# Performance work log

Hardware: AMD Instinct MI355X
Metric: run time of the kernel (lower is better)

Reference implementation:

```python
import jax, jax.numpy as jnp
import numpy as np

VOCAB, EMBED, TOPICS, NDOCS = 30000, 200, 100, 2048
DT_ALPHA, TW_ALPHA = 3.0, 2.0
EPS_OT = 1e-16   # ETP sinkhorn epsilon
EPS_LOG = 1e-12  # FASTopic self.epsilon
N_SINKHORN_ITERS = 100  # fixed iteration count (original: while err>thr and cpt<max_iter)


def pairwise_sqeuclidean(x, y):
    return (jnp.sum(x * x, axis=1, keepdims=True)
            + jnp.sum(y * y, axis=1)
            - 2.0 * (x @ y.T))


def sinkhorn_etp(x, y, a, b, alpha):
    # Entropic OT between point clouds x:[n,d], y:[m,d]; a:[n,1], b:[m,1] marginals.
    M = pairwise_sqeuclidean(x, y)          # [n, m]
    K = jnp.exp(-alpha * M)                  # Gibbs kernel
    u0 = jnp.full_like(a, 1.0 / a.shape[0])

    def step(carry, _):
        u, _v = carry
        v = b / (K.T @ u + EPS_OT)           # [m,1]
        u = a / (K @ v + EPS_OT)             # [n,1]
        return (u, v), None

    (u, v), _ = jax.lax.scan(step, (u0, jnp.zeros_like(b)), None, length=N_SINKHORN_ITERS)
    transp = u * (K * v.T)                   # [n, m] transport plan
    loss = jnp.sum(transp * M)
    return loss, transp


def setup_inputs() -> dict:
    key = jax.random.key(0)
    k1, k2, k3, k4 = jax.random.split(key, 4)
    # word_embeddings: trunc_normal(std=1) then L2-row-normalize
    we = jax.random.truncated_normal(k1, -2.0, 2.0, (VOCAB, EMBED), jnp.float32)
    we = we / jnp.linalg.norm(we, axis=1, keepdims=True)
    # topic_embeddings: trunc_normal(std=0.1) then L2-row-normalize
    te = 0.1 * jax.random.truncated_normal(k2, -2.0, 2.0, (TOPICS, EMBED), jnp.float32)
    te = te / jnp.linalg.norm(te, axis=1, keepdims=True)
    word_weights = jnp.full((VOCAB, 1), 1.0 / VOCAB, jnp.float32)
    topic_weights = jnp.full((TOPICS, 1), 1.0 / TOPICS, jnp.float32)
    train_bow = jax.random.uniform(k3, (NDOCS, VOCAB), jnp.float32)
    doc_embeddings = jax.random.normal(k4, (NDOCS, EMBED), jnp.float32)
    return {
        "train_bow": train_bow,
        "doc_embeddings": doc_embeddings,
        "word_embeddings": we,
        "topic_embeddings": te,
        "word_weights": word_weights,
        "topic_weights": topic_weights,
    }


def reference(train_bow, doc_embeddings, word_embeddings, topic_embeddings,
              word_weights, topic_weights):
    n_docs = doc_embeddings.shape[0]
    n_topics = topic_embeddings.shape[0]
    # DT_ETP: a uniform over docs, b = softmax(topic_weights)
    a_dt = jnp.full((n_docs, 1), 1.0 / n_docs, doc_embeddings.dtype)
    b_dt = jax.nn.softmax(topic_weights, axis=0)
    loss_DT, transp_DT = sinkhorn_etp(doc_embeddings, topic_embeddings, a_dt, b_dt, DT_ALPHA)
    # TW_ETP: a uniform over topics, b = softmax(word_weights)
    a_tw = jnp.full((n_topics, 1), 1.0 / n_topics, topic_embeddings.dtype)
    b_tw = jax.nn.softmax(word_weights, axis=0)
    loss_TW, transp_TW = sinkhorn_etp(topic_embeddings, word_embeddings, a_tw, b_tw, TW_ALPHA)

    loss_ETP = loss_DT + loss_TW
    theta = transp_DT * n_docs               # [N, K]
    beta = transp_TW * n_topics              # [K, V]
    recon = theta @ beta                     # [N, V]
    loss_DSR = -jnp.mean(jnp.sum(train_bow * jnp.log(recon + EPS_LOG), axis=1))
    loss = loss_DSR + loss_ETP
    return loss, loss_DSR, loss_ETP
```

## Files before the change

### kernel.cpp

```cpp
#include <hip/hip_runtime.h>
#include <math.h>

#define V 30000
#define E 200
#define T 100
#define N 2048
#define NITER 100
#define KSTR 112
#define EPS_OT 1e-16f
#define EPS_LOG 1e-12f

#define OFF_KTW    0
#define OFF_KDT    1680000
#define OFF_WW     1884800
#define OFF_DD     1914800
#define OFF_TT     1916848
#define OFF_PM     1916976
#define OFF_PS     1917104
#define OFF_BTW    1917232
#define OFF_BDT    1947232
#define OFF_ACC    1947360
#define OFF_ACCDT  1957360
#define OFF_VTW    1967360
#define OFF_UDT    1997360
#define OFF_UTW    1999408
#define OFF_VDT    1999536
#define OFF_DBL    1999664
#define OFF_FLAG   1999680
#define OFF_KDTNZ  1999681

#define LOBF(u) __uint_as_float((u) << 16)
#define HIBF(u) __uint_as_float((u) & 0xffff0000u)

__device__ __forceinline__ unsigned short f2bf(float f) {
    unsigned int u = __float_as_uint(f);
    return (unsigned short)((u + 0x7fffu + ((u >> 16) & 1u)) >> 16);
}
__device__ __forceinline__ float bf2f(unsigned short h) {
    return __uint_as_float(((unsigned int)h) << 16);
}

__device__ __forceinline__ float brsum(float x, float* red8) {
    int tid = threadIdx.x;
    for (int o = 32; o; o >>= 1) x += __shfl_down(x, o, 64);
    __syncthreads();
    if ((tid & 63) == 0) red8[tid >> 6] = x;
    __syncthreads();
    return (red8[0] + red8[1]) + (red8[2] + red8[3]);
}

__device__ __forceinline__ void load_krow(const unsigned short* kg, int j, unsigned* ku) {
    const uint4* kp = (const uint4*)(kg + (size_t)j * KSTR);
    #pragma unroll
    for (int i = 0; i < 12; i++) {
        uint4 q = kp[i];
        ku[4*i] = q.x; ku[4*i+1] = q.y; ku[4*i+2] = q.z; ku[4*i+3] = q.w;
    }
    uint2 q2 = *(const uint2*)(((const unsigned*)kp) + 48);
    ku[48] = q2.x; ku[49] = q2.y;
}

__global__ void k_pre(const float* __restrict__ we, const float* __restrict__ de,
                      const float* __restrict__ te, const float* __restrict__ wwgt,
                      const float* __restrict__ twgt, float* ws) {
    __shared__ float red[256];
    int tid = threadIdx.x, b = blockIdx.x;
    int gid = b * 256 + tid;
    if (gid < 2 * NITER * T) ws[OFF_ACC + gid] = 0.f;
    if (gid < 16) ws[OFF_DBL + gid] = 0.f;
    if (gid < 2) ((int*)ws)[OFF_FLAG + gid] = 0;
    {
        int r = gid;
        const float* src = nullptr; float* dst = nullptr; int row = 0;
        if (r < V)              { src = we; dst = ws + OFF_WW; row = r; }
        else if (r < V + N)     { src = de; dst = ws + OFF_DD; row = r - V; }
        else if (r < V + N + T) { src = te; dst = ws + OFF_TT; row = r - V - N; }
        if (src) {
            const float4* p = (const float4*)(src + (size_t)row * E);
            float s = 0.f;
            #pragma unroll 10
            for (int i = 0; i < E / 4; i++) { float4 v = p[i]; s += v.x*v.x + v.y*v.y + v.z*v.z + v.w*v.w; }
            dst[row] = s;
        }
    }
    if (b < 118) {
        int j = gid;
        float w = (j < V) ? wwgt[j] : -INFINITY;
        red[tid] = w; __syncthreads();
        for (int s = 128; s > 0; s >>= 1) { if (tid < s) red[tid] = fmaxf(red[tid], red[tid + s]); __syncthreads(); }
        float m = red[0]; __syncthreads();
        float e = (j < V) ? expf(w - m) : 0.f;
        red[tid] = e; __syncthreads();
        for (int s = 128; s > 0; s >>= 1) { if (tid < s) red[tid] += red[tid + s]; __syncthreads(); }
        if (tid == 0) { ws[OFF_PM + b] = m; ws[OFF_PS + b] = red[0]; }
    } else if (b == 120) {
        float w = (tid < T) ? twgt[tid] : -INFINITY;
        red[tid] = w; __syncthreads();
        for (int s = 128; s > 0; s >>= 1) { if (tid < s) red[tid] = fmaxf(red[tid], red[tid + s]); __syncthreads(); }
        float m = red[0]; __syncthreads();
        float e = (tid < T) ? expf(w - m) : 0.f;
        red[tid] = e; __syncthreads();
        for (int s = 128; s > 0; s >>= 1) { if (tid < s) red[tid] += red[tid + s]; __syncthreads(); }
        if (tid < T) ws[OFF_BDT + tid] = e / red[0];
    }
}

__global__ void k_pre2(const float* __restrict__ wwgt, float* ws) {
    __shared__ float red[128];
    int tid = threadIdx.x, b = blockIdx.x;
    float m = (tid < 118) ? ws[OFF_PM + tid] : -INFINITY;
    if (tid < 128) red[tid] = m;
    __syncthreads();
    for (int s = 64; s > 0; s >>= 1) { if (tid < s) red[tid] = fmaxf(red[tid], red[tid + s]); __syncthreads(); }
    float mw = red[0]; __syncthreads();
    float p = (tid < 118) ? ws[OFF_PS + tid] * expf(ws[OFF_PM + tid] - mw) : 0.f;
    if (tid < 128) red[tid] = p;
    __syncthreads();
    for (int s = 64; s > 0; s >>= 1) { if (tid < s) red[tid] += red[tid + s]; __syncthreads(); }
    float Sw = red[0];
    int j = b * 256 + tid;
    if (j < V) ws[OFF_BTW + j] = expf(wwgt[j] - mw) / Sw;
}

__global__ void k_ktw(const float* __restrict__ we, const float* __restrict__ te, float* ws) {
    __shared__ float wt[8][256];
    __shared__ float tp[8][25];
    __shared__ float tts[25];
    int tid = threadIdx.x;
    int j0 = blockIdx.x * 256;
    int t0 = blockIdx.y * 25;
    int j = j0 + tid;
    int jl = (j < V) ? j : V - 1;
    float acc[25];
    #pragma unroll
    for (int i = 0; i < 25; i++) acc[i] = 0.f;
    if (tid < 25) tts[tid] = ws[OFF_TT + t0 + tid];
    for (int kk = 0; kk < E; kk += 8) {
        #pragma unroll
        for (int k = 0; k < 8; k++) wt[k][tid] = we[(size_t)jl * E + kk + k];
        if (tid < 200) { int i = tid >> 3; int k = tid & 7; tp[k][i] = te[(size_t)(t0 + i) * E + kk + k]; }
        __syncthreads();
        #pragma unroll
        for (int k = 0; k < 8; k++) {
            float w = wt[k][tid];
            #pragma unroll
            for (int i = 0; i < 25; i++) acc[i] += tp[k][i] * w;
        }
        __syncthreads();
    }
    if (j < V) {
        float wwj = ws[OFF_WW + j];
        unsigned short* kg = (unsigned short*)(ws + OFF_KTW);
        #pragma unroll
        for (int i = 0; i < 25; i++) {
            float M = tts[i] + wwj - 2.f * acc[i];
            kg[(size_t)j * KSTR + t0 + i] = f2bf(expf(-2.f * M));
        }
    }
}

__global__ void k_kdt(const float* __restrict__ de, const float* __restrict__ te, float* ws) {
    int gid = blockIdx.x * 256 + threadIdx.x;
    if (gid >= N * T) return;
    int n = gid / T; int t = gid - n * T;
    const float4* dp  = (const float4*)(de + (size_t)n * E);
    const float4* tpp = (const float4*)(te + (size_t)t * E);
    float s = 0.f;
    #pragma unroll 10
    for (int i = 0; i < E / 4; i++) { float4 a = dp[i], b = tpp[i]; s += a.x*b.x + a.y*b.y + a.z*b.z + a.w*b.w; }
    float M = ws[OFF_DD + n] + ws[OFF_TT + t] - 2.f * s;
    float kv = expf(-3.f * M);
    ws[OFF_KDT + gid] = kv;
    unsigned long long m = __ballot(kv != 0.f);
    if (m && (threadIdx.x & 63) == 0) atomicOr(((int*)ws) + OFF_KDTNZ, 1);
}

__global__ void k_it(const float* __restrict__ bow, float* ws, int k) {
    __shared__ float sm[256 * 26];
    __shared__ float pr[256];
    __shared__ float u_sh[100];
    __shared__ float red8[8];
    int tid = threadIdx.x, b = blockIdx.x;

    if (b >= 118 && b < 246) {
        if (k >= 96) return;
        const float4* b4 = (const float4*)bow;
        size_t base = (size_t)k * 160000;
        float s = 0.f;
        for (int i = (b - 118) * 256 + tid; i < 160000; i += 128 * 256) {
            float4 x = b4[base + i]; s += (x.x + x.y) + (x.z + x.w);
        }
        float bs = brsum(s, red8);
        if (tid == 0) atomicAdd((double*)(ws + OFF_DBL) + 3, (double)bs);
        return;
    }

    if (b >= 246) {
        if (((volatile int*)ws)[OFF_KDTNZ] == 0) return;
        int d = (b - 246) * 256 + tid;
        if (tid < T) u_sh[tid] = (k == 0) ? 0.f
            : ws[OFF_BDT + tid] / (ws[OFF_ACCDT + (k - 1) * T + tid] + EPS_OT);
        __syncthreads();
        const float* Kr = ws + OFF_KDT + (size_t)d * T;
        float u;
        if (k == 0) u = 1.f / N;
        else {
            float s = 0.f;
            #pragma unroll 4
            for (int t = 0; t < T; t++) s += Kr[t] * u_sh[t];
            u = (1.f / N) / (s + EPS_OT);
        }
        #pragma unroll
        for (int c = 0; c < 4; c++) {
            #pragma unroll
            for (int i = 0; i < 25; i++) sm[tid * 26 + i] = Kr[25 * c + i] * u;
            __syncthreads();
            int g = tid >> 5, tl = tid & 31;
            float s2 = 0.f;
            if (tl < 25) {
                #pragma unroll 8
                for (int q = 0; q < 32; q++) s2 += sm[(g * 32 + q) * 26 + tl];
            }
            pr[g * 32 + tl] = s2;
            __syncthreads();
            if (tid < 25) {
                float r = 0.f;
                #pragma unroll
                for (int g2 = 0; g2 < 8; g2++) r += pr[g2 * 32 + tid];
                atomicAdd(&ws[OFF_ACCDT + k * T + 25 * c + tid], r);
            }
            __syncthreads();
        }
        return;
    }

    const unsigned short* kg = (const unsigned short*)(ws + OFF_KTW);
    int j = b * 256 + tid;
    bool oob = (j >= V);
    int jc = oob ? V - 1 : j;
    unsigned ku[50];
    load_krow(kg, jc, ku);
    if (oob) {
        #pragma unroll
        for (int q = 0; q < 50; q++) ku[q] = 0;
    }
    if (tid < T) u_sh[tid] = (k == 0) ? 0.01f
        : 0.01f / (ws[OFF_ACC + (k - 1) * T + tid] + EPS_OT);
    __syncthreads();
    float s = 0.f;
    #pragma unroll
    for (int q = 0; q < 50; q++)
        s += LOBF(ku[q]) * u_sh[2 * q] + HIBF(ku[q]) * u_sh[2 * q + 1];
    float v = oob ? 0.f : ws[OFF_BTW + j] / (s + EPS_OT);
    if (k == NITER - 1 && !oob) ws[OFF_VTW + j] = v;
    #pragma unroll
    for (int c = 0; c < 4; c++) {
        #pragma unroll
        for (int i = 0; i < 25; i++) {
            int t = 25 * c + i;
            unsigned w = ku[t >> 1];
            float kt = (t & 1) ? HIBF(w) : LOBF(w);
            sm[tid * 26 + i] = kt * v;
        }
        __syncthreads();
        int g = tid >> 5, tl = tid & 31;
        float s2 = 0.f;
        if (tl < 25) {
            #pragma unroll 8
            for (int q = 0; q < 32; q++) s2 += sm[(g * 32 + q) * 26 + tl];
        }
        pr[g * 32 + tl] = s2;
        __syncthreads();
        if (tid < 25) {
            float r = 0.f;
            #pragma unroll
            for (int g2 = 0; g2 < 8; g2++) r += pr[g2 * 32 + tid];
            atomicAdd(&ws[OFF_ACC + k * T + 25 * c + tid], r);
        }
        __syncthreads();
    }
}

__global__ void k_post(float* ws) {
    __shared__ float u_sh[100];
    __shared__ float red8[8];
    int tid = threadIdx.x, b = blockIdx.x;
    if (b < 118) {
        if (tid < T) {
            float uf = 0.01f / (ws[OFF_ACC + (NITER - 1) * T + tid] + EPS_OT);
            u_sh[tid] = uf;
            if (b == 0) ws[OFF_UTW + tid] = uf;
        }
        __syncthreads();
        int j = b * 256 + tid;
        float lt = 0.f;
        if (j < V) {
            const unsigned short* kg = (const unsigned short*)(ws + OFF_KTW);
            unsigned ku[50];
            load_krow(kg, j, ku);
            float v = ws[OFF_VTW + j];
            #pragma unroll
            for (int q = 0; q < 50; q++) {
                float k0 = LOBF(ku[q]), k1 = HIBF(ku[q]);
                if (k0 > 0.f) lt += u_sh[2 * q]     * k0 * v * (-0.5f * logf(k0));
                if (k1 > 0.f) lt += u_sh[2 * q + 1] * k1 * v * (-0.5f * logf(k1));
            }
        }
        float ltb = brsum(lt, red8);
        if (tid == 0) atomicAdd((double*)(ws + OFF_DBL) + 2, (double)ltb);
    } else {
        if (((volatile int*)ws)[OFF_KDTNZ] == 0) return;
        if (tid < T) {
            float vf = ws[OFF_BDT + tid] / (ws[OFF_ACCDT + (NITER - 1) * T + tid] + EPS_OT);
            u_sh[tid] = vf;
            if (b == 118) ws[OFF_VDT + tid] = vf;
        }
        __syncthreads();
        int d = (b - 118) * 256 + tid;
        const float* Kr = ws + OFF_KDT + (size_t)d * T;
        float s = 0.f;
        #pragma unroll 4
        for (int t = 0; t < T; t++) s += Kr[t] * u_sh[t];
        float u = (1.f / N) / (s + EPS_OT);
        ws[OFF_UDT + d] = u;
        float ld = 0.f; int nz = 0;
        for (int t = 0; t < T; t++) {
            float kv = Kr[t];
            if (kv > 0.f) ld += u * kv * u_sh[t] * (-(1.f / 3.f) * logf(kv));
            if ((float)N * u * kv * u_sh[t] != 0.f) nz = 1;
        }
        float ldb = brsum(ld, red8);
        if (tid == 0) atomicAdd((double*)(ws + OFF_DBL) + 1, (double)ldb);
        if (nz) atomicOr(((int*)ws) + OFF_FLAG, 1);
    }
}

__global__ void k_dsr(const float* __restrict__ bow, float* ws) {
    if (*(volatile int*)(((int*)ws) + OFF_FLAG) == 0) return;
    __shared__ float th[32 * T];
    __shared__ float u2[T];
    __shared__ float vd[T];
    __shared__ float red[256];
    __shared__ int flag;
    int tid = threadIdx.x;
    int j0 = blockIdx.x * 256;
    int d0 = blockIdx.y * 32;
    if (tid < T) { vd[tid] = ws[OFF_VDT + tid]; u2[tid] = ws[OFF_UTW + tid]; }
    if (tid == 0) flag = 0;
    __syncthreads();
    bool nz = false;
    for (int idx = tid; idx < 32 * T; idx += 256) {
        int dl = idx / T; int t = idx - dl * T;
        float thv = (float)N * ws[OFF_UDT + d0 + dl] * ws[OFF_KDT + (size_t)(d0 + dl) * T + t] * vd[t];
        th[idx] = thv;
        nz |= (thv != 0.f);
    }
    if (nz) flag = 1;
    __syncthreads();
    int j = j0 + tid;
    float part = 0.f;
    const unsigned short* kg = (const unsigned short*)(ws + OFF_KTW);
    if (flag) {
        float acc[32];
        #pragma unroll
        for (int d = 0; d < 32; d++) acc[d] = 0.f;
        if (j < V) {
            float vj = ws[OFF_VTW + j];
            for (int t = 0; t < T; t++) {
                float kv = bf2f(kg[(size_t)j * KSTR + t]);
                float beta = (float)T * u2[t] * kv * vj;
                #pragma unroll
                for (int d = 0; d < 32; d++) acc[d] += th[d * T + t] * beta;
            }
            for (int d = 0; d < 32; d++)
                part += bow[(size_t)(d0 + d) * V + j] * logf(acc[d] + EPS_LOG);
        }
    } else {
        if (j < V) {
            float sb = 0.f;
            #pragma unroll 8
            for (int d = 0; d < 32; d++) sb += bow[(size_t)(d0 + d) * V + j];
            part = sb * logf(EPS_LOG);
        }
    }
    red[tid] = part; __syncthreads();
    for (int s = 128; s > 0; s >>= 1) { if (tid < s) red[tid] += red[tid + s]; __syncthreads(); }
    if (tid == 0) atomicAdd((double*)(ws + OFF_DBL) + 0, (double)red[0]);
}

__global__ void k_finish(float* ws, float* out) {
    if (threadIdx.x == 0 && blockIdx.x == 0) {
        double* dbl = (double*)(ws + OFF_DBL);
        int flag = ((int*)ws)[OFF_FLAG];
        double dsr_sum = flag ? dbl[0] : dbl[3] * (double)logf(EPS_LOG);
        double ldsr = -dsr_sum / (double)N;
        double letp = dbl[1] + dbl[2];
        out[0] = (float)(ldsr + letp);
        out[1] = (float)ldsr;
        out[2] = (float)letp;
    }
}

extern "C" void kernel_launch(void* const* d_in, const int* in_sizes, int n_in,
                              void* d_out, int out_size, void* d_ws, size_t ws_size,
                              hipStream_t stream) {
    const float* bow  = (const float*)d_in[0];
    const float* de   = (const float*)d_in[1];
    const float* we   = (const float*)d_in[2];
    const float* te   = (const float*)d_in[3];
    const float* wwgt = (const float*)d_in[4];
    const float* twgt = (const float*)d_in[5];
    float* out = (float*)d_out;
    float* ws  = (float*)d_ws;

    k_pre<<<128, 256, 0, stream>>>(we, de, te, wwgt, twgt, ws);
    k_pre2<<<118, 256, 0, stream>>>(wwgt, ws);
    k_ktw<<<dim3(118, 4), 256, 0, stream>>>(we, te, ws);
    k_kdt<<<800, 256, 0, stream>>>(de, te, ws);
    for (int k = 0; k < NITER; k++)
        k_it<<<254, 256, 0, stream>>>(bow, ws, k);
    k_post<<<126, 256, 0, stream>>>(ws);
    k_dsr<<<dim3(118, 64), 256, 0, stream>>>(bow, ws);
    k_finish<<<1, 64, 0, stream>>>(ws, out);
}
```

Baseline: 1.314 ms.

## Fuse Sinkhorn iterations into one persistent kernel with grid barriers

Replaces the 100 per-iteration k_it launches and the k_post launch with a single persistent kernel, k_sink. The TW and DT block groups each loop over the iterations and synchronise through separate atomic-counter grid barriers. TW blocks keep their K rows in registers across iterations instead of reloading them each launch, and the post-processing is folded into the tail. This removes launch overhead and repeated K reloads, but relies on all 254 blocks being co-resident; otherwise the spin barriers could deadlock.

```diff
diff --git a/kernel.cpp b/kernel.cpp
--- a/kernel.cpp
+++ b/kernel.cpp
@@ -28,6 +28,10 @@
 #define OFF_DBL    1999664
 #define OFF_FLAG   1999680
 #define OFF_KDTNZ  1999681
+#define OFF_ARR    1999682
+
+#define NTW 118
+#define NDT 8
 
 #define LOBF(u) __uint_as_float((u) << 16)
 #define HIBF(u) __uint_as_float((u) & 0xffff0000u)
@@ -58,6 +62,20 @@
     }
     uint2 q2 = *(const uint2*)(((const unsigned*)kp) + 48);
     ku[48] = q2.x; ku[49] = q2.y;
+}
+
+__device__ __forceinline__ void gbar(int* ctr, int n, int tid) {
+    __syncthreads();
+    if (tid == 0) {
+        __hip_atomic_fetch_add(ctr, 1, __ATOMIC_RELEASE, __HIP_MEMORY_SCOPE_AGENT);
+        while (__hip_atomic_load(ctr, __ATOMIC_ACQUIRE, __HIP_MEMORY_SCOPE_AGENT) < n)
+            __builtin_amdgcn_s_sleep(1);
+    }
+    __syncthreads();
+}
+
+__device__ __forceinline__ float agent_ldf(const float* p) {
+    return __hip_atomic_load(p, __ATOMIC_RELAXED, __HIP_MEMORY_SCOPE_AGENT);
 }
 
 __global__ void k_pre(const float* __restrict__ we, const float* __restrict__ de,
@@ -69,6 +87,7 @@
     if (gid < 2 * NITER * T) ws[OFF_ACC + gid] = 0.f;
     if (gid < 16) ws[OFF_DBL + gid] = 0.f;
     if (gid < 2) ((int*)ws)[OFF_FLAG + gid] = 0;
+    if (gid < 2 * NITER) ((int*)ws)[OFF_ARR + gid] = 0;
     {
         int r = gid;
         const float* src = nullptr; float* dst = nullptr; int row = 0;
@@ -175,149 +194,73 @@
     if (m && (threadIdx.x & 63) == 0) atomicOr(((int*)ws) + OFF_KDTNZ, 1);
 }
 
-__global__ void k_it(const float* __restrict__ bow, float* ws, int k) {
+__global__ __launch_bounds__(256, 1) void k_sink(const float* __restrict__ bow, float* ws) {
     __shared__ float sm[256 * 26];
     __shared__ float pr[256];
     __shared__ float u_sh[100];
     __shared__ float red8[8];
     int tid = threadIdx.x, b = blockIdx.x;
+    int* arr = ((int*)ws) + OFF_ARR;
 
     if (b >= 118 && b < 246) {
-        if (k >= 96) return;
         const float4* b4 = (const float4*)bow;
-        size_t base = (size_t)k * 160000;
-        float s = 0.f;
-        for (int i = (b - 118) * 256 + tid; i < 160000; i += 128 * 256) {
-            float4 x = b4[base + i]; s += (x.x + x.y) + (x.z + x.w);
-        }
-        float bs = brsum(s, red8);
-        if (tid == 0) atomicAdd((double*)(ws + OFF_DBL) + 3, (double)bs);
+        for (int k = 0; k < 96; k++) {
+            size_t base = (size_t)k * 160000;
+            float s = 0.f;
+            for (int i = (b - 118) * 256 + tid; i < 160000; i += 128 * 256) {
+                float4 x = b4[base + i]; s += (x.x + x.y) + (x.z + x.w);
+            }
+            float bs = brsum(s, red8);
+            if (tid == 0) atomicAdd((double*)(ws + OFF_DBL) + 3, (double)bs);
+        }
         return;
     }
 
     if (b >= 246) {
         if (((volatile int*)ws)[OFF_KDTNZ] == 0) return;
         int d = (b - 246) * 256 + tid;
-        if (tid < T) u_sh[tid] = (k == 0) ? 0.f
-            : ws[OFF_BDT + tid] / (ws[OFF_ACCDT + (k - 1) * T + tid] + EPS_OT);
+        const float* Kr = ws + OFF_KDT + (size_t)d * T;
+        for (int k = 0; k < NITER; k++) {
+            if (tid < T) u_sh[tid] = (k == 0) ? 0.f
+                : ws[OFF_BDT + tid] / (agent_ldf(ws + OFF_ACCDT + (k - 1) * T + tid) + EPS_OT);
+            __syncthreads();
+            float u;
+            if (k == 0) u = 1.f / N;
+            else {
+                float s = 0.f;
+                #pragma unroll 4
+                for (int t = 0; t < T; t++) s += Kr[t] * u_sh[t];
+                u = (1.f / N) / (s + EPS_OT);
+            }
+            #pragma unroll
+            for (int c = 0; c < 4; c++) {
+                #pragma unroll
+                for (int i = 0; i < 25; i++) sm[tid * 26 + i] = Kr[25 * c + i] * u;
+                __syncthreads();
+                int g = tid >> 5, tl = tid & 31;
+                float s2 = 0.f;
+                if (tl < 25) {
+                    #pragma unroll 8
+                    for (int q = 0; q < 32; q++) s2 += sm[(g * 32 + q) * 26 + tl];
+                }
+                pr[g * 32 + tl] = s2;
+                __syncthreads();
+                if (tid < 25) {
+                    float r = 0.f;
+                    #pragma unroll
+                    for (int g2 = 0; g2 < 8; g2++) r += pr[g2 * 32 + tid];
+                    atomicAdd(&ws[OFF_ACCDT + k * T + 25 * c + tid], r);
+                }
+                __syncthreads();
+            }
+            gbar(arr + NITER + k, NDT, tid);
+        }
+        if (tid < T) {
+            float vf = ws[OFF_BDT + tid] / (agent_ldf(ws + OFF_ACCDT + (NITER - 1) * T + tid) + EPS_OT);
+            u_sh[tid] = vf;
+            if (b == 246) ws[OFF_VDT + tid] = vf;
+        }
         __syncthreads();
-        const float* Kr = ws + OFF_KDT + (size_t)d * T;
-        float u;
-        if (k == 0) u = 1.f / N;
-        else {
-            float s = 0.f;
-            #pragma unroll 4
-            for (int t = 0; t < T; t++) s += Kr[t] * u_sh[t];
-            u = (1.f / N) / (s + EPS_OT);
-        }
-        #pragma unroll
-        for (int c = 0; c < 4; c++) {
-            #pragma unroll
-            for (int i = 0; i < 25; i++) sm[tid * 26 + i] = Kr[25 * c + i] * u;
-            __syncthreads();
-            int g = tid >> 5, tl = tid & 31;
-            float s2 = 0.f;
-            if (tl < 25) {
-                #pragma unroll 8
-                for (int q = 0; q < 32; q++) s2 += sm[(g * 32 + q) * 26 + tl];
-            }
-            pr[g * 32 + tl] = s2;
-            __syncthreads();
-            if (tid < 25) {
-                float r = 0.f;
-                #pragma unroll
-                for (int g2 = 0; g2 < 8; g2++) r += pr[g2 * 32 + tid];
-                atomicAdd(&ws[OFF_ACCDT + k * T + 25 * c + tid], r);
-            }
-            __syncthreads();
-        }
-        return;
-    }
-
-    const unsigned short* kg = (const unsigned short*)(ws + OFF_KTW);
-    int j = b * 256 + tid;
-    bool oob = (j >= V);
-    int jc = oob ? V - 1 : j;
-    unsigned ku[50];
-    load_krow(kg, jc, ku);
-    if (oob) {
-        #pragma unroll
-        for (int q = 0; q < 50; q++) ku[q] = 0;
-    }
-    if (tid < T) u_sh[tid] = (k == 0) ? 0.01f
-        : 0.01f / (ws[OFF_ACC + (k - 1) * T + tid] + EPS_OT);
-    __syncthreads();
-    float s = 0.f;
-    #pragma unroll
-    for (int q = 0; q < 50; q++)
-        s += LOBF(ku[q]) * u_sh[2 * q] + HIBF(ku[q]) * u_sh[2 * q + 1];
-    float v = oob ? 0.f : ws[OFF_BTW + j] / (s + EPS_OT);
-    if (k == NITER - 1 && !oob) ws[OFF_VTW + j] = v;
-    #pragma unroll
-    for (int c = 0; c < 4; c++) {
-        #pragma unroll
-        for (int i = 0; i < 25; i++) {
-            int t = 25 * c + i;
-            unsigned w = ku[t >> 1];
-            float kt = (t & 1) ? HIBF(w) : LOBF(w);
-            sm[tid * 26 + i] = kt * v;
-        }
-        __syncthreads();
-        int g = tid >> 5, tl = tid & 31;
-        float s2 = 0.f;
-        if (tl < 25) {
-            #pragma unroll 8
-            for (int q = 0; q < 32; q++) s2 += sm[(g * 32 + q) * 26 + tl];
-        }
-        pr[g * 32 + tl] = s2;
-        __syncthreads();
-        if (tid < 25) {
-            float r = 0.f;
-            #pragma unroll
-            for (int g2 = 0; g2 < 8; g2++) r += pr[g2 * 32 + tid];
-            atomicAdd(&ws[OFF_ACC + k * T + 25 * c + tid], r);
-        }
-        __syncthreads();
-    }
-}
-
-__global__ void k_post(float* ws) {
-    __shared__ float u_sh[100];
-    __shared__ float red8[8];
-    int tid = threadIdx.x, b = blockIdx.x;
-    if (b < 118) {
-        if (tid < T) {
-            float uf = 0.01f / (ws[OFF_ACC + (NITER - 1) * T + tid] + EPS_OT);
-            u_sh[tid] = uf;
-            if (b == 0) ws[OFF_UTW + tid] = uf;
-        }
-        __syncthreads();
-        int j = b * 256 + tid;
-        float lt = 0.f;
-        if (j < V) {
-            const unsigned short* kg = (const unsigned short*)(ws + OFF_KTW);
-            unsigned ku[50];
-            load_krow(kg, j, ku);
-            float v = ws[OFF_VTW + j];
-            #pragma unroll
-            for (int q = 0; q < 50; q++) {
-                float k0 = LOBF(ku[q]), k1 = HIBF(ku[q]);
-                if (k0 > 0.f) lt += u_sh[2 * q]     * k0 * v * (-0.5f * logf(k0));
-                if (k1 > 0.f) lt += u_sh[2 * q + 1] * k1 * v * (-0.5f * logf(k1));
-            }
-        }
-        float ltb = brsum(lt, red8);
-        if (tid == 0) atomicAdd((double*)(ws + OFF_DBL) + 2, (double)ltb);
-    } else {
-        if (((volatile int*)ws)[OFF_KDTNZ] == 0) return;
-        if (tid < T) {
-            float vf = ws[OFF_BDT + tid] / (ws[OFF_ACCDT + (NITER - 1) * T + tid] + EPS_OT);
-            u_sh[tid] = vf;
-            if (b == 118) ws[OFF_VDT + tid] = vf;
-        }
-        __syncthreads();
-        int d = (b - 118) * 256 + tid;
-        const float* Kr = ws + OFF_KDT + (size_t)d * T;
         float s = 0.f;
         #pragma unroll 4
         for (int t = 0; t < T; t++) s += Kr[t] * u_sh[t];
@@ -332,7 +275,78 @@
         float ldb = brsum(ld, red8);
         if (tid == 0) atomicAdd((double*)(ws + OFF_DBL) + 1, (double)ldb);
         if (nz) atomicOr(((int*)ws) + OFF_FLAG, 1);
-    }
+        return;
+    }
+
+    const unsigned short* kg = (const unsigned short*)(ws + OFF_KTW);
+    int j = b * 256 + tid;
+    bool oob = (j >= V);
+    int jc = oob ? V - 1 : j;
+    unsigned ku[50];
+    load_krow(kg, jc, ku);
+    if (oob) {
+        #pragma unroll
+        for (int q = 0; q < 50; q++) ku[q] = 0;
+    }
+    float bj = oob ? 0.f : ws[OFF_BTW + j];
+    float v = 0.f;
+    for (int k = 0; k < NITER; k++) {
+        if (tid < T) u_sh[tid] = (k == 0) ? 0.01f
+            : 0.01f / (agent_ldf(ws + OFF_ACC + (k - 1) * T + tid) + EPS_OT);
+        __syncthreads();
+        float s = 0.f;
+        #pragma unroll
+        for (int q = 0; q < 50; q++)
+            s += LOBF(ku[q]) * u_sh[2 * q] + HIBF(ku[q]) * u_sh[2 * q + 1];
+        v = oob ? 0.f : bj / (s + EPS_OT);
+        if (k == NITER - 1 && !oob) ws[OFF_VTW + j] = v;
+        __syncthreads();
+        #pragma unroll
+        for (int c = 0; c < 4; c++) {
+            #pragma unroll
+            for (int i = 0; i < 25; i++) {
+                int t = 25 * c + i;
+                unsigned w = ku[t >> 1];
+                float kt = (t & 1) ? HIBF(w) : LOBF(w);
+                sm[tid * 26 + i] = kt * v;
+            }
+            __syncthreads();
+            int g = tid >> 5, tl = tid & 31;
+            float s2 = 0.f;
+            if (tl < 25) {
+                #pragma unroll 8
+                for (int q = 0; q < 32; q++) s2 += sm[(g * 32 + q) * 26 + tl];
+            }
+            pr[g * 32 + tl] = s2;
+            __syncthreads();
+            if (tid < 25) {
+                float r = 0.f;
+                #pragma unroll
+                for (int g2 = 0; g2 < 8; g2++) r += pr[g2 * 32 + tid];
+                atomicAdd(&ws[OFF_ACC + k * T + 25 * c + tid], r);
+            }
+            __syncthreads();
+        }
+        gbar(arr + k, NTW, tid);
+    }
+    if (tid < T) {
+        float a = agent_ldf(ws + OFF_ACC + (NITER - 1) * T + tid);
+        float uf = 0.01f / (a + EPS_OT);
+        u_sh[tid] = uf;
+        if (b == 0) ws[OFF_UTW + tid] = uf;
+    }
+    __syncthreads();
+    float lt = 0.f;
+    if (!oob) {
+        #pragma unroll
+        for (int q = 0; q < 50; q++) {
+            float k0 = LOBF(ku[q]), k1 = HIBF(ku[q]);
+            if (k0 > 0.f) lt += u_sh[2 * q]     * k0 * v * (-0.5f * logf(k0));
+            if (k1 > 0.f) lt += u_sh[2 * q + 1] * k1 * v * (-0.5f * logf(k1));
+        }
+    }
+    float ltb = brsum(lt, red8);
+    if (tid == 0) atomicAdd((double*)(ws + OFF_DBL) + 2, (double)ltb);
 }
 
 __global__ void k_dsr(const float* __restrict__ bow, float* ws) {
@@ -417,9 +431,7 @@
     k_pre2<<<118, 256, 0, stream>>>(wwgt, ws);
     k_ktw<<<dim3(118, 4), 256, 0, stream>>>(we, te, ws);
     k_kdt<<<800, 256, 0, stream>>>(de, te, ws);
-    for (int k = 0; k < NITER; k++)
-        k_it<<<254, 256, 0, stream>>>(bow, ws, k);
-    k_post<<<126, 256, 0, stream>>>(ws);
+    k_sink<<<254, 256, 0, stream>>>(bow, ws);
     k_dsr<<<dim3(118, 64), 256, 0, stream>>>(bow, ws);
     k_finish<<<1, 64, 0, stream>>>(ws, out);
 }
```

After: 1.395 ms. 6.1% more time.
